# Optimization experiments

Measured on AMD Instinct MI355X. Metric: run time of the kernel, lower is better.

The kernel has to match this reference:

```python
import jax, jax.numpy as jnp
import numpy as np


def setup_inputs() -> dict:
    key = jax.random.key(0)
    k1, k2, k3 = jax.random.split(key, 3)
    B, T, D, U = 32, 2048, 512, 512
    x = jax.random.normal(k1, (B, T, D), dtype=jnp.float32)
    W = jax.random.normal(k2, (D, U), dtype=jnp.float32) * (1.0 / np.sqrt(D))
    R = jax.random.normal(k3, (U, U), dtype=jnp.float32) * (1.0 / np.sqrt(U))
    h0 = jnp.zeros((B, U), dtype=jnp.float32)
    return {"x": x, "W": W, "R": R, "h0": h0}


def reference(x, W, R, h0):
    # Linear recurrence: h_t = x_t @ W + h_{t-1} @ R
    # Precompute the input projection for all timesteps in one big GEMM.
    xW = jnp.einsum("btd,du->btu", x, W)  # [B, T, U]

    def step(h, xw_t):
        h_new = xw_t + h @ R  # [B, U]
        return h_new, h_new

    # scan over time (leading axis): move T to front
    _, hs = jax.lax.scan(step, h0, jnp.swapaxes(xW, 0, 1))  # hs: [T, B, U]
    return jnp.swapaxes(hs, 0, 1)  # [B, T, U]
```

## Files before the change

### kernel.cpp

```cpp
#include <hip/hip_runtime.h>
#include <hip/hip_bf16.h>


typedef float f32x4 __attribute__((ext_vector_type(4)));
typedef __bf16 bf16x8 __attribute__((ext_vector_type(8)));

#define TDIM 2048L
#define UDIM 512L
#define ST32 16384L
#define ST64 32768L
#define TS 262144L
#define FE 786432L
#define PP 520

__device__ __forceinline__ f32x4 mfma16(bf16x8 a, bf16x8 b, f32x4 c) {
  return __builtin_amdgcn_mfma_f32_16x16x32_bf16(a, b, c, 0, 0, 0);
}

__device__ __forceinline__ int hidx(int row, int col) {
  return row * 512 + (col ^ ((row & 7) << 3));
}

__device__ __forceinline__ void pack8(const f32x4& v0, const f32x4& v1,
                                      bf16x8& hv, bf16x8& lv) {
#pragma unroll
  for (int j = 0; j < 4; ++j) {
    const float a = v0[j];
    const __bf16 ha = (__bf16)a;
    hv[j] = ha; lv[j] = (__bf16)(a - (float)ha);
    const float b = v1[j];
    const __bf16 hb = (__bf16)b;
    hv[j + 4] = hb; lv[j + 4] = (__bf16)(b - (float)hb);
  }
}


__device__ __forceinline__ void stage32p(const float* __restrict__ src,
                                         long pitch, __bf16* Phi, __bf16* Plo) {
  for (int i = threadIdx.x; i < 2048; i += blockDim.x) {
    const int row = i >> 6, cb = i & 63;
    const float* p = src + (long)row * pitch + cb * 8;
    bf16x8 hv, lv;
    pack8(*(const f32x4*)p, *(const f32x4*)(p + 4), hv, lv);
    const int o = row * PP + cb * 8;
    *(bf16x8*)(Phi + o) = hv;
    *(bf16x8*)(Plo + o) = lv;
  }
}

__device__ __forceinline__ void write_bt(const __bf16* Phi, const __bf16* Plo,
                                         float* out, long t) {
  for (int i = threadIdx.x; i < 2048; i += blockDim.x) {
    const int row = i >> 6, cb = i & 63;
    const int o = row * PP + cb * 8;
    const bf16x8 hv = *(const bf16x8*)(Phi + o);
    const bf16x8 lv = *(const bf16x8*)(Plo + o);
    f32x4 o0, o1;
#pragma unroll
    for (int j = 0; j < 4; ++j) {
      o0[j] = (float)hv[j] + (float)lv[j];
      o1[j] = (float)hv[j + 4] + (float)lv[j + 4];
    }
    float* dst = out + (long)row * (TDIM * UDIM) + t * UDIM + cb * 8;
    *(f32x4*)dst = o0;
    *(f32x4*)(dst + 4) = o1;
  }
}

__device__ __forceinline__ void write_flat(const __bf16* Phi, const __bf16* Plo,
                                           float* dst) {
  for (int i = threadIdx.x; i < 2048; i += blockDim.x) {
    const int row = i >> 6, cb = i & 63;
    const int o = row * PP + cb * 8;
    const bf16x8 hv = *(const bf16x8*)(Phi + o);
    const bf16x8 lv = *(const bf16x8*)(Plo + o);
    f32x4 o0, o1;
#pragma unroll
    for (int j = 0; j < 4; ++j) {
      o0[j] = (float)hv[j] + (float)lv[j];
      o1[j] = (float)hv[j + 4] + (float)lv[j + 4];
    }
    float* d = dst + row * 512 + cb * 8;
    *(f32x4*)d = o0;
    *(f32x4*)(d + 4) = o1;
  }
}

template <int NTERM, int NPROD, bool HAS_H>
__device__ __forceinline__ void pstep32(__bf16* Phi, __bf16* Plo,
                                        const __bf16* __restrict__ bfrag,
                                        const float* __restrict__ xwbase, long t) {
  const int tid = threadIdx.x, l = tid & 63, w = tid >> 6, g = l >> 4, li = l & 15;
  f32x4 addv[2][2];
#pragma unroll
  for (int mt = 0; mt < 2; ++mt)
#pragma unroll
    for (int q = 0; q < 2; ++q) {
      const int col = (w * 2 + q) * 16 + li;
#pragma unroll
      for (int r = 0; r < 4; ++r) {
        const int bat = mt * 16 + g * 4 + r;
        addv[mt][q][r] = xwbase[(long)bat * (TDIM * UDIM) + t * UDIM + col];
      }
    }

  f32x4 acc[2][2] = {};
  if (HAS_H) {
#pragma unroll 2
    for (int kk = 0; kk < 16; ++kk) {
      bf16x8 b[NTERM][2];
#pragma unroll
      for (int q = 0; q < 2; ++q) {
        const long fo = (((long)(w * 2 + q) * 16 + kk) * 64 + l) * 8;
#pragma unroll
        for (int tt = 0; tt < NTERM; ++tt)
          b[tt][q] = *(const bf16x8*)(bfrag + (long)tt * TS + fo);
      }
#pragma unroll
      for (int mt = 0; mt < 2; ++mt) {
        const int o = (mt * 16 + li) * PP + kk * 32 + g * 8;
        const bf16x8 a1 = *(const bf16x8*)(Phi + o);
        const bf16x8 a2 = *(const bf16x8*)(Plo + o);
#pragma unroll
        for (int q = 0; q < 2; ++q) {
          acc[mt][q] = mfma16(a1, b[0][q], acc[mt][q]);
          acc[mt][q] = mfma16(a1, b[1][q], acc[mt][q]);
          if (NPROD >= 3) acc[mt][q] = mfma16(a2, b[0][q], acc[mt][q]);
          if (NPROD >= 4) acc[mt][q] = mfma16(a1, b[NTERM - 1][q], acc[mt][q]);
        }
      }
    }
    __syncthreads();
  }

#pragma unroll
  for (int mt = 0; mt < 2; ++mt)
#pragma unroll
    for (int q = 0; q < 2; ++q) {
      const int col = (w * 2 + q) * 16 + li;
#pragma unroll
      for (int r = 0; r < 4; ++r) {
        const float v = (HAS_H ? acc[mt][q][r] : 0.0f) + addv[mt][q][r];
        const int row = mt * 16 + g * 4 + r;
        const __bf16 hi = (__bf16)v;
        const int o = row * PP + col;
        Phi[o] = hi;
        Plo[o] = (__bf16)(v - (float)hi);
      }
    }
  __syncthreads();
}

__device__ __forceinline__ void dstep(__bf16* Phi, __bf16* Plo,
                                      __bf16* Qhi, __bf16* Qlo,
                                      const __bf16* __restrict__ r2f,
                                      const __bf16* __restrict__ rf,
                                      const float* __restrict__ xw,
                                      long t1, long t2) {
  stage32p(xw + t1 * UDIM, TDIM * UDIM, Qhi, Qlo);
  __syncthreads();
  const int tid = threadIdx.x, l = tid & 63, w = tid >> 6, g = l >> 4, li = l & 15;
  f32x4 addv[2][2];
#pragma unroll
  for (int mt = 0; mt < 2; ++mt)
#pragma unroll
    for (int q = 0; q < 2; ++q) {
      const int col = (w * 2 + q) * 16 + li;
#pragma unroll
      for (int r = 0; r < 4; ++r) {
        const int bat = mt * 16 + g * 4 + r;
        addv[mt][q][r] = xw[(long)bat * (TDIM * UDIM) + t2 * UDIM + col];
      }
    }
  f32x4 acc[2][2] = {};
#pragma unroll 2
  for (int kk = 0; kk < 16; ++kk) {
    bf16x8 c0[2], c1[2], d0[2], d1[2];
#pragma unroll
    for (int q = 0; q < 2; ++q) {
      const long fo = (((long)(w * 2 + q) * 16 + kk) * 64 + l) * 8;
      c0[q] = *(const bf16x8*)(r2f + fo);
      c1[q] = *(const bf16x8*)(r2f + TS + fo);
      d0[q] = *(const bf16x8*)(rf + fo);
      d1[q] = *(const bf16x8*)(rf + TS + fo);
    }
#pragma unroll
    for (int mt = 0; mt < 2; ++mt) {
      const int o = (mt * 16 + li) * PP + kk * 32 + g * 8;
      const bf16x8 h1 = *(const bf16x8*)(Phi + o);
      const bf16x8 h2 = *(const bf16x8*)(Plo + o);
      const bf16x8 q1 = *(const bf16x8*)(Qhi + o);
      const bf16x8 q2 = *(const bf16x8*)(Qlo + o);
#pragma unroll
      for (int q = 0; q < 2; ++q) {
        acc[mt][q] = mfma16(h1, c0[q], acc[mt][q]);
        acc[mt][q] = mfma16(q1, d0[q], acc[mt][q]);
        acc[mt][q] = mfma16(h1, c1[q], acc[mt][q]);
        acc[mt][q] = mfma16(q1, d1[q], acc[mt][q]);
        acc[mt][q] = mfma16(h2, c0[q], acc[mt][q]);
        acc[mt][q] = mfma16(q2, d0[q], acc[mt][q]);
      }
    }
  }
  __syncthreads();
#pragma unroll
  for (int mt = 0; mt < 2; ++mt)
#pragma unroll
    for (int q = 0; q < 2; ++q) {
      const int col = (w * 2 + q) * 16 + li;
#pragma unroll
      for (int r = 0; r < 4; ++r) {
        const float v = acc[mt][q][r] + addv[mt][q][r];
        const int row = mt * 16 + g * 4 + r;
        const __bf16 hi = (__bf16)v;
        const int o = row * PP + col;
        Phi[o] = hi;
        Plo[o] = (__bf16)(v - (float)hi);
      }
    }
  __syncthreads();
}


__device__ __forceinline__ void xw_dev(long blk, const float* __restrict__ x,
                                       const __bf16* __restrict__ wf,
                                       float* __restrict__ out, char* smem) {
  __bf16* Phi = (__bf16*)smem;
  const float* src = x + blk * ST64;
  for (int i = threadIdx.x; i < 4096; i += 512) {
    const int row = i >> 6, cb = i & 63;
    const f32x4 v0 = *(const f32x4*)(src + (long)row * 512 + cb * 8);
    const f32x4 v1 = *(const f32x4*)(src + (long)row * 512 + cb * 8 + 4);
    bf16x8 hv;
#pragma unroll
    for (int j = 0; j < 4; ++j) {
      hv[j] = (__bf16)v0[j];
      hv[j + 4] = (__bf16)v1[j];
    }
    *(bf16x8*)(Phi + row * PP + cb * 8) = hv;
  }
  __syncthreads();
  const int tid = threadIdx.x, l = tid & 63, w = tid >> 6, g = l >> 4, li = l & 15;
  f32x4 acc[4][4] = {};
#pragma unroll 2
  for (int kk = 0; kk < 16; ++kk) {
    bf16x8 b0[4], b1[4];
#pragma unroll
    for (int q = 0; q < 4; ++q) {
      const long fo = (((long)(w * 4 + q) * 16 + kk) * 64 + l) * 8;
      b0[q] = *(const bf16x8*)(wf + fo);
      b1[q] = *(const bf16x8*)(wf + TS + fo);
    }
#pragma unroll
    for (int mt = 0; mt < 4; ++mt) {
      const bf16x8 a1 = *(const bf16x8*)(Phi + (mt * 16 + li) * PP + kk * 32 + g * 8);
#pragma unroll
      for (int q = 0; q < 4; ++q) {
        acc[mt][q] = mfma16(a1, b0[q], acc[mt][q]);
        acc[mt][q] = mfma16(a1, b1[q], acc[mt][q]);
      }
    }
  }
  float* gdst = out + blk * ST64;
#pragma unroll
  for (int mt = 0; mt < 4; ++mt)
#pragma unroll
    for (int q = 0; q < 4; ++q) {
      const int col = (w * 4 + q) * 16 + li;
#pragma unroll
      for (int r = 0; r < 4; ++r)
        gdst[(long)(mt * 16 + g * 4 + r) * 512 + col] = acc[mt][q][r];
    }
}

__device__ __forceinline__ void stage_sw(const float* __restrict__ src,
                                         float* hbuf) {
  for (int i = threadIdx.x; i < 4096; i += 512) {
    const int flat = i * 4, row = flat >> 9, col = flat & 511;
    *(f32x4*)&hbuf[hidx(row, col)] = *(const f32x4*)&src[flat];
  }
}

__device__ __forceinline__ f32x4 lds_mm(const float* hbuf,
                                        const __bf16* __restrict__ bf,
                                        int mt, int ntg) {
  const int tid = threadIdx.x, l = tid & 63, g = (l >> 4) & 3, li = l & 15;
  f32x4 acc = {};
#pragma unroll 2
  for (int kk = 0; kk < 16; ++kk) {
    const long fo = (((long)ntg * 16 + kk) * 64 + l) * 8;
    const bf16x8 b0 = *(const bf16x8*)(bf + fo);
    const bf16x8 b1 = *(const bf16x8*)(bf + TS + fo);
    bf16x8 a1, a2;
    const float* pp = &hbuf[hidx(mt * 16 + li, kk * 32 + g * 8)];
#pragma unroll
    for (int j = 0; j < 8; ++j) {
      const float v = pp[j];
      const __bf16 hi = (__bf16)v;
      a1[j] = hi;
      a2[j] = (__bf16)(v - (float)hi);
    }
    acc = mfma16(a1, b0, acc);
    acc = mfma16(a1, b1, acc);
    acc = mfma16(a2, b0, acc);
  }
  return acc;
}

__device__ __forceinline__ void sq_dev(int b, const float* __restrict__ a,
                                       const __bf16* __restrict__ bf,
                                       float* __restrict__ of32,
                                       __bf16* __restrict__ ofr, float* hbuf) {
  const int rg = b >> 3, cg = b & 7;
  const int tid = threadIdx.x, l = tid & 63, w = tid >> 6, g = l >> 4, li = l & 15;
  stage_sw(a + (long)rg * ST32, hbuf);
  __syncthreads();
  const int mt = w >> 2, q = w & 3, ntg = cg * 4 + q;
  f32x4 acc = {};
#pragma unroll 2
  for (int kk = 0; kk < 16; ++kk) {
    const long fo = (((long)ntg * 16 + kk) * 64 + l) * 8;
    const bf16x8 b0 = *(const bf16x8*)(bf + fo);
    const bf16x8 b1 = *(const bf16x8*)(bf + TS + fo);
    const bf16x8 b2 = *(const bf16x8*)(bf + 2 * TS + fo);
    bf16x8 a1, a2;
    const float* pp = &hbuf[hidx(mt * 16 + li, kk * 32 + g * 8)];
#pragma unroll
    for (int j = 0; j < 8; ++j) {
      const float v = pp[j];
      const __bf16 hi = (__bf16)v;
      a1[j] = hi;
      a2[j] = (__bf16)(v - (float)hi);
    }
    acc = mfma16(a1, b0, acc);
    acc = mfma16(a1, b1, acc);
    acc = mfma16(a2, b0, acc);
    acc = mfma16(a1, b2, acc);
  }
  const int n = ntg * 16 + li;
#pragma unroll
  for (int r = 0; r < 4; ++r) {
    const int k = rg * 32 + mt * 16 + g * 4 + r;
    const float v = acc[r];
    of32[(long)k * 512 + n] = v;
    const __bf16 t1 = (__bf16)v;
    const float r1 = v - (float)t1;
    const __bf16 t2 = (__bf16)r1;
    const long fi = (((long)(n >> 4) * 16 + (k >> 5)) * 64 + ((k >> 3) & 3) * 16 + (n & 15)) * 8 + (k & 7);
    ofr[fi] = t1;
    ofr[TS + fi] = t2;
    ofr[2 * TS + fi] = (__bf16)(r1 - (float)t2);
  }
}

__device__ __forceinline__ void pair_dev(int b, const float* __restrict__ in,
                                         const __bf16* __restrict__ bf,
                                         float* __restrict__ outb, float* hbuf) {
  const int p = b >> 3, cs = b & 7;
  const int tid = threadIdx.x, l = tid & 63, w = tid >> 6, g = l >> 4, li = l & 15;
  stage_sw(in + (long)(2 * p) * ST32, hbuf);
  __syncthreads();
  const int mt = w >> 2, ntg = cs * 4 + (w & 3);
  const f32x4 acc = lds_mm(hbuf, bf, mt, ntg);
  const float* addp = in + (long)(2 * p + 1) * ST32;
  float* outp = outb + (long)p * ST32;
  const int col = ntg * 16 + li;
#pragma unroll
  for (int r = 0; r < 4; ++r) {
    const int row = mt * 16 + g * 4 + r;
    outp[(long)row * 512 + col] = acc[r] + addp[(long)row * 512 + col];
  }
}


__global__ __launch_bounds__(512) void k_split2(const float* __restrict__ m0,
                                                const float* __restrict__ m1,
                                                __bf16* __restrict__ f0,
                                                __bf16* __restrict__ f1) {
  const int bb = blockIdx.x;
  const float* m = (bb < 512) ? m0 : m1;
  __bf16* f = (bb < 512) ? f0 : f1;
  const int idx = (bb & 511) * 512 + threadIdx.x;
  const int j = idx & 7, l = (idx >> 3) & 63, kk = (idx >> 9) & 15, nt = idx >> 13;
  const int k = kk * 32 + (l >> 4) * 8 + j;
  const int n = nt * 16 + (l & 15);
  const float v = m[k * 512 + n];
  const __bf16 t1 = (__bf16)v;
  const float r1 = v - (float)t1;
  const __bf16 t2 = (__bf16)r1;
  f[idx] = t1;
  f[TS + idx] = t2;
  f[2 * TS + idx] = (__bf16)(r1 - (float)t2);
}

__global__ __launch_bounds__(512) void k_xw(const float* __restrict__ x,
                                            const __bf16* __restrict__ wf,
                                            float* __restrict__ out, int base) {
  __shared__ __align__(16) char smem[64 * PP * 2];
  xw_dev(base + blockIdx.x, x, wf, out, smem);
}

__global__ __launch_bounds__(512) void k_xwsq(const float* __restrict__ sqa,
                                              const __bf16* __restrict__ sqbf,
                                              float* __restrict__ sqo32,
                                              __bf16* __restrict__ sqofr,
                                              const float* __restrict__ x,
                                              const __bf16* __restrict__ wf,
                                              float* __restrict__ out, int base) {
  __shared__ __align__(16) char smem[64 * PP * 2];
  const int b = blockIdx.x;
  if (b < 128)
    sq_dev(b, sqa, sqbf, sqo32, sqofr, (float*)smem);
  else
    xw_dev(base + (b - 128), x, wf, out, smem);
}

__global__ __launch_bounds__(512) void k_combo(const float* __restrict__ sqa,
                                               const __bf16* __restrict__ sqbf,
                                               float* __restrict__ sqo32,
                                               __bf16* __restrict__ sqofr,
                                               const float* __restrict__ prin,
                                               const __bf16* __restrict__ prbf,
                                               float* __restrict__ prout) {
  __shared__ float hbuf[ST32];
  const int b = blockIdx.x;
  if (b < 128)
    sq_dev(b, sqa, sqbf, sqo32, sqofr, hbuf);
  else
    pair_dev(b - 128, prin, prbf, prout, hbuf);
}

__global__ __launch_bounds__(1024) void k_local(const float* __restrict__ xw,
                                                const __bf16* __restrict__ rf,
                                                const __bf16* __restrict__ r2f,
                                                float* __restrict__ sout) {
  __shared__ __bf16 Phi[32 * PP], Plo[32 * PP], Qhi[32 * PP], Qlo[32 * PP];
  const long c = blockIdx.x;
  stage32p(xw + c * 8 * UDIM, TDIM * UDIM, Phi, Plo);
  __syncthreads();
  pstep32<2, 3, true>(Phi, Plo, rf, xw, c * 8 + 1);
  dstep(Phi, Plo, Qhi, Qlo, r2f, rf, xw, c * 8 + 2, c * 8 + 3);
  dstep(Phi, Plo, Qhi, Qlo, r2f, rf, xw, c * 8 + 4, c * 8 + 5);
  dstep(Phi, Plo, Qhi, Qlo, r2f, rf, xw, c * 8 + 6, c * 8 + 7);
  write_flat(Phi, Plo, sout + c * ST32);
}

__global__ __launch_bounds__(1024) void k_fix0(const float* __restrict__ e0,
                                               float* out,
                                               const __bf16* __restrict__ rf) {
  __shared__ __bf16 Phi[32 * PP], Plo[32 * PP];
  const long c = blockIdx.x;
  stage32p(e0 + c * ST32, 512, Phi, Plo);
  __syncthreads();
  for (int j = 0; j < 8; ++j) {
    pstep32<2, 3, true>(Phi, Plo, rf, out, c * 8 + j);
    write_bt(Phi, Plo, out, c * 8 + j);
  }
}

__global__ __launch_bounds__(512) void k_down(const float* __restrict__ epar,
                                              float* __restrict__ ulev,
                                              const __bf16* __restrict__ bf) {
  __shared__ float hbuf[ST32];
  const int p = blockIdx.x >> 3, cs = blockIdx.x & 7;
  const int tid = threadIdx.x, l = tid & 63, w = tid >> 6, g = l >> 4, li = l & 15;
  stage_sw(epar + (long)p * ST32, hbuf);
  __syncthreads();
  const int mt = w >> 2, ntg = cs * 4 + (w & 3);
  const f32x4 acc = lds_mm(hbuf, bf, mt, ntg);
  float* evp = ulev + (long)(2 * p) * ST32;
  float* outp = ulev + (long)(2 * p + 1) * ST32;
  const int col = ntg * 16 + li;
  float cp[4];
#pragma unroll
  for (int r = 0; r < 4; ++r) {
    const int row = mt * 16 + g * 4 + r;
    const long off = (long)row * 512 + col;
    cp[r] = hbuf[hidx(row, col)];
    outp[off] = acc[r] + evp[off];
  }
  __syncthreads();
#pragma unroll
  for (int r = 0; r < 4; ++r) {
    const int row = mt * 16 + g * 4 + r;
    evp[(long)row * 512 + col] = cp[r];
  }
}

extern "C" void kernel_launch(void* const* d_in, const int* in_sizes, int n_in,
                              void* d_out, int out_size, void* d_ws, size_t ws_size,
                              hipStream_t stream) {
  (void)in_sizes; (void)n_in; (void)out_size; (void)ws_size;
  const float* x  = (const float*)d_in[0];
  const float* W  = (const float*)d_in[1];
  const float* R  = (const float*)d_in[2];
  const float* h0 = (const float*)d_in[3];
  float* out = (float*)d_out;

  __bf16* F  = (__bf16*)d_ws;
  __bf16* Fw = F + 11 * FE;
  float* P1 = (float*)(Fw + FE);
  float* P2 = P1 + TS;
  float* Sbuf = P2 + TS;
  float* Ub[8];
  {
    float* up = Sbuf + 256 * ST32;
    for (int k = 1; k <= 7; ++k) { Ub[k] = up; up += (1L << (8 - k)) * ST32; }
  }

  k_split2<<<1024, 512, 0, stream>>>(W, R, Fw, F);

  k_xwsq<<<384, 512, 0, stream>>>(R, F, P1, F + FE, x, Fw, out, 0);
  k_xwsq<<<384, 512, 0, stream>>>(P1, F + FE, P2, F + 2L * FE, x, Fw, out, 256);
  k_xwsq<<<384, 512, 0, stream>>>(P2, F + 2L * FE, P1, F + 3L * FE, x, Fw, out, 512);
  k_xw<<<256, 512, 0, stream>>>(x, Fw, out, 768);

  k_local<<<256, 1024, 0, stream>>>(out, F, F + FE, Sbuf);

  for (int k = 1; k <= 7; ++k) {
    const int i = k + 3;
    const float* sqa = (i & 1) ? P2 : P1;
    float* sqo = (i & 1) ? P1 : P2;
    const float* prin = (k == 1) ? Sbuf : Ub[k - 1];
    const int npr = (1 << (8 - k)) * 8;
    k_combo<<<128 + npr, 512, 0, stream>>>(sqa, F + (long)(i - 1) * FE, sqo,
                                           F + (long)i * FE, prin,
                                           F + (long)(k + 2) * FE, Ub[k]);
  }

  k_down<<<8, 512, 0, stream>>>(h0, Ub[7], F + 10L * FE);
  for (int k = 7; k >= 1; --k) {
    float* ul = (k == 1) ? Sbuf : Ub[k - 1];
    k_down<<<(1 << (8 - k)) * 8, 512, 0, stream>>>(Ub[k], ul, F + (long)(k + 2) * FE);
  }

  k_fix0<<<256, 1024, 0, stream>>>(Sbuf, out, F);
}
```

Measured before the change: 521.0 us.

## Fold last down-sweep level into fix kernel and drop low-part W MFMA

The final k_down level is removed. Its work moves into k_fix0: odd blocks first apply one R^8 step to the parent state before running the eight local R steps. This saves a kernel launch and a global round trip through Sbuf. The xW projection GEMM now multiplies only by the high bf16 part of W, skipping the low-part correction term. That halves the MFMA and weight loads in that GEMM at some cost in accuracy. The unroll factors of the k-loops also rise from 2 to 4.

Result: faster. 488.7 us (-6.2%).

```diff
diff --git a/kernel.cpp b/kernel.cpp
--- a/kernel.cpp
+++ b/kernel.cpp
@@ -89,7 +89,8 @@
 template <int NTERM, int NPROD, bool HAS_H>
 __device__ __forceinline__ void pstep32(__bf16* Phi, __bf16* Plo,
                                         const __bf16* __restrict__ bfrag,
-                                        const float* __restrict__ xwbase, long t) {
+                                        const float* __restrict__ addbase,
+                                        long addpitch) {
   const int tid = threadIdx.x, l = tid & 63, w = tid >> 6, g = l >> 4, li = l & 15;
   f32x4 addv[2][2];
 #pragma unroll
@@ -100,13 +101,13 @@
 #pragma unroll
       for (int r = 0; r < 4; ++r) {
         const int bat = mt * 16 + g * 4 + r;
-        addv[mt][q][r] = xwbase[(long)bat * (TDIM * UDIM) + t * UDIM + col];
+        addv[mt][q][r] = addbase[(long)bat * addpitch + col];
       }
     }
 
   f32x4 acc[2][2] = {};
   if (HAS_H) {
-#pragma unroll 2
+#pragma unroll 4
     for (int kk = 0; kk < 16; ++kk) {
       bf16x8 b[NTERM][2];
 #pragma unroll
@@ -242,23 +243,20 @@
   __syncthreads();
   const int tid = threadIdx.x, l = tid & 63, w = tid >> 6, g = l >> 4, li = l & 15;
   f32x4 acc[4][4] = {};
-#pragma unroll 2
+#pragma unroll 4
   for (int kk = 0; kk < 16; ++kk) {
-    bf16x8 b0[4], b1[4];
+    bf16x8 b0[4];
 #pragma unroll
     for (int q = 0; q < 4; ++q) {
       const long fo = (((long)(w * 4 + q) * 16 + kk) * 64 + l) * 8;
       b0[q] = *(const bf16x8*)(wf + fo);
-      b1[q] = *(const bf16x8*)(wf + TS + fo);
     }
 #pragma unroll
     for (int mt = 0; mt < 4; ++mt) {
       const bf16x8 a1 = *(const bf16x8*)(Phi + (mt * 16 + li) * PP + kk * 32 + g * 8);
 #pragma unroll
-      for (int q = 0; q < 4; ++q) {
+      for (int q = 0; q < 4; ++q)
         acc[mt][q] = mfma16(a1, b0[q], acc[mt][q]);
-        acc[mt][q] = mfma16(a1, b1[q], acc[mt][q]);
-      }
     }
   }
   float* gdst = out + blk * ST64;
@@ -438,22 +436,26 @@
   const long c = blockIdx.x;
   stage32p(xw + c * 8 * UDIM, TDIM * UDIM, Phi, Plo);
   __syncthreads();
-  pstep32<2, 3, true>(Phi, Plo, rf, xw, c * 8 + 1);
+  pstep32<2, 3, true>(Phi, Plo, rf, xw + (c * 8 + 1) * UDIM, TDIM * UDIM);
   dstep(Phi, Plo, Qhi, Qlo, r2f, rf, xw, c * 8 + 2, c * 8 + 3);
   dstep(Phi, Plo, Qhi, Qlo, r2f, rf, xw, c * 8 + 4, c * 8 + 5);
   dstep(Phi, Plo, Qhi, Qlo, r2f, rf, xw, c * 8 + 6, c * 8 + 7);
   write_flat(Phi, Plo, sout + c * ST32);
 }
 
-__global__ __launch_bounds__(1024) void k_fix0(const float* __restrict__ e0,
+__global__ __launch_bounds__(1024) void k_fix0(const float* __restrict__ e1,
+                                               const float* __restrict__ sbuf,
                                                float* out,
-                                               const __bf16* __restrict__ rf) {
+                                               const __bf16* __restrict__ rf,
+                                               const __bf16* __restrict__ r8f) {
   __shared__ __bf16 Phi[32 * PP], Plo[32 * PP];
   const long c = blockIdx.x;
-  stage32p(e0 + c * ST32, 512, Phi, Plo);
-  __syncthreads();
+  stage32p(e1 + (c >> 1) * ST32, 512, Phi, Plo);
+  __syncthreads();
+  if (c & 1)
+    pstep32<2, 3, true>(Phi, Plo, r8f, sbuf + (c - 1) * ST32, 512);
   for (int j = 0; j < 8; ++j) {
-    pstep32<2, 3, true>(Phi, Plo, rf, out, c * 8 + j);
+    pstep32<2, 3, true>(Phi, Plo, rf, out + (c * 8 + j) * UDIM, TDIM * UDIM);
     write_bt(Phi, Plo, out, c * 8 + j);
   }
 }
@@ -529,10 +531,8 @@
   }
 
   k_down<<<8, 512, 0, stream>>>(h0, Ub[7], F + 10L * FE);
-  for (int k = 7; k >= 1; --k) {
-    float* ul = (k == 1) ? Sbuf : Ub[k - 1];
-    k_down<<<(1 << (8 - k)) * 8, 512, 0, stream>>>(Ub[k], ul, F + (long)(k + 2) * FE);
-  }
-
-  k_fix0<<<256, 1024, 0, stream>>>(Sbuf, out, F);
-}
+  for (int k = 7; k >= 2; --k)
+    k_down<<<(1 << (8 - k)) * 8, 512, 0, stream>>>(Ub[k], Ub[k - 1], F + (long)(k + 2) * FE);
+
+  k_fix0<<<256, 1024, 0, stream>>>(Ub[1], Sbuf, out, F, F + 3L * FE);
+}
```
